# Performance work log

Measured on AMD Instinct MI355X. Metric: run time of the kernel, lower is better.

The kernel has to match this reference:

```python
import jax, jax.numpy as jnp
import numpy as np

CW = 64            # channel_width; N = CW**2 = 4096 tokens = d_batch
BIAS = 1.0         # same_channel_bias
D_KQ = 2048
D_V = 2048
STEP = 0           # self.step at first call
T_IDX = 0          # self.t at first call
PE_N = 10000.0


def pe_row(t, d, n=PE_N):
    """Row t of the sinusoidal positional encoding P[t, :] of width d (d even)."""
    i = jnp.arange(d // 2, dtype=jnp.float32)
    denom = jnp.power(jnp.float32(n), 2.0 * i / d)
    ang = jnp.float32(t) / denom
    row = jnp.zeros((d,), dtype=jnp.float32)
    row = row.at[0::2].set(jnp.sin(ang)).at[1::2].set(jnp.cos(ang))
    return row


def setup_inputs() -> dict:
    key = jax.random.key(0)
    ks = jax.random.split(key, 6)
    N = CW * CW          # 4096
    d_in = 2048
    num_steps = 8
    return {
        "x": jax.random.normal(ks[0], (N, d_in), dtype=jnp.float32),
        "W_query": jax.random.uniform(ks[1], (d_in, D_KQ), dtype=jnp.float32),
        "W_key": jax.random.uniform(ks[2], (d_in, D_KQ), dtype=jnp.float32),
        "W_value": jax.random.uniform(ks[3], (d_in, D_V), dtype=jnp.float32),
        "b_channel": jax.random.uniform(ks[4], (N, D_V), dtype=jnp.float32),
        "b_t": jax.random.uniform(ks[5], (num_steps, N, D_V), dtype=jnp.float32),
    }


def reference(x, W_query, W_key, W_value, b_channel, b_t):
    N = x.shape[0]
    q = x @ W_query                      # [N, d_kq]
    k = x @ W_key                        # [N, d_kq]
    v = x @ W_value                      # [N, d_v]
    scores = q @ k.T                     # [N, N]
    # kron(eye(cw), ones(cw,cw)*bias): +bias where tokens share a channel block
    ch = jnp.arange(N) // CW
    scores = scores + jnp.where(ch[:, None] == ch[None, :], jnp.float32(BIAS), jnp.float32(0.0))
    # NOTE: bias added BEFORE the 1/sqrt(d_kq) scaling, as in the original
    attn = jax.nn.softmax(scores / jnp.float32(D_KQ) ** 0.5, axis=-1)
    ctx = attn @ v                       # [N, d_v]
    ctx = ctx + b_channel + b_t[STEP] + pe_row(T_IDX, D_V)
    return ctx
```

## Files before the change

kernel.cpp:

```cpp
#include <hip/hip_runtime.h>
#include <cstdint>
#include <cstddef>


using h8    = __attribute__((ext_vector_type(8))) _Float16;
using h4    = __attribute__((ext_vector_type(4))) _Float16;
using f32x4 = __attribute__((ext_vector_type(4))) float;

__device__ __forceinline__ void gll16(const void* g, void* l) {
  __builtin_amdgcn_global_load_lds(
      (const __attribute__((address_space(1))) uint32_t*)g,
      (__attribute__((address_space(3))) uint32_t*)l, 16, 0, 0);
}

__global__ __launch_bounds__(256) void split_x_kernel(
    const float* __restrict__ X, _Float16* __restrict__ hi,
    _Float16* __restrict__ lo, int n4)
{
  int i = blockIdx.x * 256 + threadIdx.x;
  if (i >= n4) return;
  float4 v = ((const float4*)X)[i];
  float a[4] = {v.x, v.y, v.z, v.w};
  h4 hh, ll;
#pragma unroll
  for (int e = 0; e < 4; ++e) {
    _Float16 h = (_Float16)a[e];
    hh[e] = h;
    ll[e] = (_Float16)(a[e] - (float)h);
  }
  ((h4*)hi)[i] = hh;
  ((h4*)lo)[i] = ll;
}

__global__ __launch_bounds__(256) void transpose_split_w(
    const float* __restrict__ W, _Float16* __restrict__ Thi,
    _Float16* __restrict__ Tlo, int D, int writeLo)
{
  __shared__ float t[32][33];
  int n0 = blockIdx.x * 32;
  int k0 = blockIdx.y * 32;
  int tx = threadIdx.x & 31;
  int ty = threadIdx.x >> 5;
  for (int j = ty; j < 32; j += 8)
    t[j][tx] = W[(size_t)(k0 + j) * D + n0 + tx];
  __syncthreads();
  for (int j = ty; j < 32; j += 8) {
    float v = t[tx][j];
    size_t o = (size_t)(n0 + j) * D + k0 + tx;
    _Float16 h = (_Float16)v;
    Thi[o] = h;
    if (writeLo) Tlo[o] = (_Float16)(v - (float)h);
  }
}

constexpr int EPI_QK = 0;
constexpr int EPI_VT = 1;
constexpr int EPI_S  = 2;
constexpr int EPI_CTX = 3;

template<int EPI, bool SPLIT>
__global__ __launch_bounds__(256, 2) void gemm_bt(
    const _Float16* __restrict__ A, const _Float16* __restrict__ Al,
    const _Float16* __restrict__ B, const _Float16* __restrict__ Bl,
    int K, int lda, int ldb, int ldc, int ldt,
    float* __restrict__ of32, _Float16* __restrict__ oh1,
    _Float16* __restrict__ oh2,
    const float* __restrict__ c1, const float* __restrict__ c2)
{
  __shared__ __align__(16) _Float16 sA [128 * 32];
  __shared__ __align__(16) _Float16 sB [128 * 32];
  __shared__ __align__(16) _Float16 sAl[SPLIT ? 128 * 32 : 8];
  __shared__ __align__(16) _Float16 sBl[SPLIT ? 128 * 32 : 8];

  const int tid  = threadIdx.x;
  const int lane = tid & 63;
  const int wave = tid >> 6;
  const int wm = wave >> 1, wn = wave & 1;
  const int m0 = blockIdx.y * 128, n0 = blockIdx.x * 128;

  const int ca = lane + 64 * wave;
  const int ra = ca >> 2, ka = (ca & 3) * 8;
  const int cc = ca + 256;
  const int rb = cc >> 2, kb = (cc & 3) * 8;
  const size_t lo0 = (size_t)wave * 1024;
  const size_t lo1 = lo0 + 4096;

  const _Float16* gA0 = A + (size_t)(m0 + ra) * lda + ka;
  const _Float16* gA1 = A + (size_t)(m0 + rb) * lda + kb;
  const _Float16* gB0 = B + (size_t)(n0 + ra) * ldb + ka;
  const _Float16* gB1 = B + (size_t)(n0 + rb) * ldb + kb;
  const _Float16* gAl0 = Al ? Al + (size_t)(m0 + ra) * lda + ka : nullptr;
  const _Float16* gAl1 = Al ? Al + (size_t)(m0 + rb) * lda + kb : nullptr;
  const _Float16* gBl0 = Bl ? Bl + (size_t)(n0 + ra) * ldb + ka : nullptr;
  const _Float16* gBl1 = Bl ? Bl + (size_t)(n0 + rb) * ldb + kb : nullptr;

  f32x4 acc[4][4];
#pragma unroll
  for (int i = 0; i < 4; ++i)
#pragma unroll
    for (int j = 0; j < 4; ++j) acc[i][j] = (f32x4){0.f, 0.f, 0.f, 0.f};

  const int fr = lane & 15;
  const int fk = (lane >> 4) * 8;

  for (int k0 = 0; k0 < K; k0 += 32) {
    gll16(gA0 + k0, (char*)sA + lo0);
    gll16(gA1 + k0, (char*)sA + lo1);
    gll16(gB0 + k0, (char*)sB + lo0);
    gll16(gB1 + k0, (char*)sB + lo1);
    if constexpr (SPLIT) {
      gll16(gAl0 + k0, (char*)sAl + lo0);
      gll16(gAl1 + k0, (char*)sAl + lo1);
      gll16(gBl0 + k0, (char*)sBl + lo0);
      gll16(gBl1 + k0, (char*)sBl + lo1);
    }
    __syncthreads();

    h8 af[4], bf[4], afl[4], bfl[4];
#pragma unroll
    for (int mi = 0; mi < 4; ++mi)
      af[mi] = *(const h8*)&sA[(wm * 64 + mi * 16 + fr) * 32 + fk];
#pragma unroll
    for (int ni = 0; ni < 4; ++ni)
      bf[ni] = *(const h8*)&sB[(wn * 64 + ni * 16 + fr) * 32 + fk];
    if constexpr (SPLIT) {
#pragma unroll
      for (int mi = 0; mi < 4; ++mi)
        afl[mi] = *(const h8*)&sAl[(wm * 64 + mi * 16 + fr) * 32 + fk];
#pragma unroll
      for (int ni = 0; ni < 4; ++ni)
        bfl[ni] = *(const h8*)&sBl[(wn * 64 + ni * 16 + fr) * 32 + fk];
    }

#pragma unroll
    for (int mi = 0; mi < 4; ++mi)
#pragma unroll
      for (int ni = 0; ni < 4; ++ni) {
        acc[mi][ni] = __builtin_amdgcn_mfma_f32_16x16x32_f16(
            af[mi], bf[ni], acc[mi][ni], 0, 0, 0);
        if constexpr (SPLIT) {
          acc[mi][ni] = __builtin_amdgcn_mfma_f32_16x16x32_f16(
              af[mi], bfl[ni], acc[mi][ni], 0, 0, 0);
          acc[mi][ni] = __builtin_amdgcn_mfma_f32_16x16x32_f16(
              afl[mi], bf[ni], acc[mi][ni], 0, 0, 0);
        }
      }
    __syncthreads();
  }

  const int drow = (lane >> 4) * 4;
  const int dcol = lane & 15;
#pragma unroll
  for (int mi = 0; mi < 4; ++mi) {
#pragma unroll
    for (int ni = 0; ni < 4; ++ni) {
      const int row = m0 + wm * 64 + mi * 16 + drow;
      const int col = n0 + wn * 64 + ni * 16 + dcol;
      f32x4 v = acc[mi][ni];
      if constexpr (EPI == EPI_S) {
#pragma unroll
        for (int r = 0; r < 4; ++r)
          of32[(size_t)(row + r) * ldc + col] = v[r];
      } else if constexpr (EPI == EPI_QK) {
#pragma unroll
        for (int r = 0; r < 4; ++r) {
          float x = v[r];
          _Float16 hh = (_Float16)x;
          size_t o = (size_t)(row + r) * ldc + col;
          oh1[o] = hh;
          oh2[o] = (_Float16)(x - (float)hh);
        }
      } else if constexpr (EPI == EPI_VT) {
        h4 hh;
#pragma unroll
        for (int r = 0; r < 4; ++r) hh[r] = (_Float16)v[r];
        *(h4*)&oh1[(size_t)col * ldt + row] = hh;
      } else {
#pragma unroll
        for (int r = 0; r < 4; ++r) {
          size_t o = (size_t)(row + r) * ldc + col;
          of32[o] = v[r] + c1[o] + c2[o] + ((col & 1) ? 1.0f : 0.0f);
        }
      }
    }
  }
}

__global__ __launch_bounds__(256) void softmax_bias_kernel(
    float* __restrict__ S, int N)
{
  const float scale = 0.022097086912079608f;
  const int row = blockIdx.x;
  float* rp = S + (size_t)row * N;
  const int cblk = row & ~63;
  const int tid = threadIdx.x;

  float vals[16];
  float mx = -3.0e38f;
#pragma unroll
  for (int it = 0; it < 4; ++it) {
    int base = (it * 256 + tid) * 4;
    float4 v = *(const float4*)(rp + base);
    float a[4] = {v.x, v.y, v.z, v.w};
#pragma unroll
    for (int e = 0; e < 4; ++e) {
      int col = base + e;
      float s = a[e];
      if ((col & ~63) == cblk) s += 1.0f;
      s *= scale;
      vals[it * 4 + e] = s;
      mx = fmaxf(mx, s);
    }
  }
  __shared__ float red[8];
#pragma unroll
  for (int m = 32; m; m >>= 1) mx = fmaxf(mx, __shfl_xor(mx, m, 64));
  if ((tid & 63) == 0) red[tid >> 6] = mx;
  __syncthreads();
  mx = fmaxf(fmaxf(red[0], red[1]), fmaxf(red[2], red[3]));

  float sum = 0.f;
#pragma unroll
  for (int i = 0; i < 16; ++i) {
    float e = __expf(vals[i] - mx);
    vals[i] = e;
    sum += e;
  }
#pragma unroll
  for (int m = 32; m; m >>= 1) sum += __shfl_xor(sum, m, 64);
  if ((tid & 63) == 0) red[4 + (tid >> 6)] = sum;
  __syncthreads();
  sum = red[4] + red[5] + red[6] + red[7];
  float inv = 1.0f / sum;

  _Float16* op = (_Float16*)rp;
#pragma unroll
  for (int it = 0; it < 4; ++it) {
    int base = (it * 256 + tid) * 4;
    h4 hh;
#pragma unroll
    for (int e = 0; e < 4; ++e) hh[e] = (_Float16)(vals[it * 4 + e] * inv);
    *(h4*)(op + base) = hh;
  }
}

extern "C" void kernel_launch(void* const* d_in, const int* in_sizes, int n_in,
                              void* d_out, int out_size, void* d_ws,
                              size_t ws_size, hipStream_t stream)
{
  (void)in_sizes; (void)n_in; (void)out_size; (void)ws_size;
  const float* x   = (const float*)d_in[0];
  const float* Wq  = (const float*)d_in[1];
  const float* Wk  = (const float*)d_in[2];
  const float* Wv  = (const float*)d_in[3];
  const float* bch = (const float*)d_in[4];
  const float* bt0 = (const float*)d_in[5];
  float* out = (float*)d_out;

  char* ws = (char*)d_ws;
  const size_t O_XHI = 0;
  const size_t O_XLO = O_XHI + 16777216;
  const size_t O_WQH = O_XLO + 16777216;
  const size_t O_WQL = O_WQH + 8388608;
  const size_t O_WKH = O_WQL + 8388608;
  const size_t O_WKL = O_WKH + 8388608;
  const size_t O_S   = 0;
  const size_t O_WVH = 67108864;
  const size_t O_VT  = O_WVH + 8388608;
  const size_t O_QH  = O_VT + 16777216;
  const size_t O_QL  = O_QH + 16777216;
  const size_t O_KH  = O_QL + 16777216;
  const size_t O_KL  = O_KH + 16777216;

  _Float16* xhi = (_Float16*)(ws + O_XHI);
  _Float16* xlo = (_Float16*)(ws + O_XLO);
  _Float16* wqh = (_Float16*)(ws + O_WQH);
  _Float16* wql = (_Float16*)(ws + O_WQL);
  _Float16* wkh = (_Float16*)(ws + O_WKH);
  _Float16* wkl = (_Float16*)(ws + O_WKL);
  _Float16* wvh = (_Float16*)(ws + O_WVH);
  _Float16* vT  = (_Float16*)(ws + O_VT);
  _Float16* qh  = (_Float16*)(ws + O_QH);
  _Float16* ql  = (_Float16*)(ws + O_QL);
  _Float16* kh  = (_Float16*)(ws + O_KH);
  _Float16* kl  = (_Float16*)(ws + O_KL);
  float*    S   = (float*)(ws + O_S);

  split_x_kernel<<<2097152 / 256, 256, 0, stream>>>(x, xhi, xlo, 2097152);
  dim3 tg(64, 64);
  transpose_split_w<<<tg, 256, 0, stream>>>(Wq, wqh, wql, 2048, 1);
  transpose_split_w<<<tg, 256, 0, stream>>>(Wk, wkh, wkl, 2048, 1);
  transpose_split_w<<<tg, 256, 0, stream>>>(Wv, wvh, nullptr, 2048, 0);

  dim3 g1(2048 / 128, 4096 / 128);
  gemm_bt<EPI_QK, true><<<g1, 256, 0, stream>>>(
      xhi, xlo, wqh, wql, 2048, 2048, 2048, 2048, 0,
      nullptr, qh, ql, nullptr, nullptr);
  gemm_bt<EPI_QK, true><<<g1, 256, 0, stream>>>(
      xhi, xlo, wkh, wkl, 2048, 2048, 2048, 2048, 0,
      nullptr, kh, kl, nullptr, nullptr);
  gemm_bt<EPI_VT, false><<<g1, 256, 0, stream>>>(
      xhi, nullptr, wvh, nullptr, 2048, 2048, 2048, 0, 4096,
      nullptr, vT, nullptr, nullptr, nullptr);

  dim3 g2(4096 / 128, 4096 / 128);
  gemm_bt<EPI_S, true><<<g2, 256, 0, stream>>>(
      qh, ql, kh, kl, 2048, 2048, 2048, 4096, 0,
      S, nullptr, nullptr, nullptr, nullptr);

  softmax_bias_kernel<<<4096, 256, 0, stream>>>(S, 4096);

  gemm_bt<EPI_CTX, false><<<g1, 256, 0, stream>>>(
      (const _Float16*)S, nullptr, vT, nullptr, 4096, 8192, 4096, 2048, 0,
      out, nullptr, nullptr, bch, bt0);
}
```

Before: 956.7 us.

## Fuse Q/K projection GEMMs, re-layout LDS tiles, raise occupancy, compact attention buffer

Concatenates the transposed Wq and Wk weights so one GEMM launch produces Q and K side by side. The attention-score GEMM then reads them with stride 4096. The LDS staging layout changes from row-major 32-wide rows to k-chunk-major blocks of 8 halves, which changes how fragments are read and may reduce bank conflicts. Launch bounds rise to 4 or 6 blocks per CU. Softmax now writes its fp16 output to a separate compact buffer, so the context GEMM reads it with lda 4096 instead of a strided view inside S. The higher occupancy target may force register spills.

```diff
diff --git a/kernel.cpp b/kernel.cpp
--- a/kernel.cpp
+++ b/kernel.cpp
@@ -59,7 +59,7 @@
 constexpr int EPI_CTX = 3;
 
 template<int EPI, bool SPLIT>
-__global__ __launch_bounds__(256, 2) void gemm_bt(
+__global__ __launch_bounds__(256, SPLIT ? 4 : 6) void gemm_bt(
     const _Float16* __restrict__ A, const _Float16* __restrict__ Al,
     const _Float16* __restrict__ B, const _Float16* __restrict__ Bl,
     int K, int lda, int ldb, int ldc, int ldt,
@@ -78,21 +78,18 @@
   const int wm = wave >> 1, wn = wave & 1;
   const int m0 = blockIdx.y * 128, n0 = blockIdx.x * 128;
 
-  const int ca = lane + 64 * wave;
-  const int ra = ca >> 2, ka = (ca & 3) * 8;
-  const int cc = ca + 256;
-  const int rb = cc >> 2, kb = (cc & 3) * 8;
+  const int s0 = wave * 64 + lane;
+  const int r  = s0 & 127;
+  const int j0 = s0 >> 7;
   const size_t lo0 = (size_t)wave * 1024;
   const size_t lo1 = lo0 + 4096;
 
-  const _Float16* gA0 = A + (size_t)(m0 + ra) * lda + ka;
-  const _Float16* gA1 = A + (size_t)(m0 + rb) * lda + kb;
-  const _Float16* gB0 = B + (size_t)(n0 + ra) * ldb + ka;
-  const _Float16* gB1 = B + (size_t)(n0 + rb) * ldb + kb;
-  const _Float16* gAl0 = Al ? Al + (size_t)(m0 + ra) * lda + ka : nullptr;
-  const _Float16* gAl1 = Al ? Al + (size_t)(m0 + rb) * lda + kb : nullptr;
-  const _Float16* gBl0 = Bl ? Bl + (size_t)(n0 + ra) * ldb + ka : nullptr;
-  const _Float16* gBl1 = Bl ? Bl + (size_t)(n0 + rb) * ldb + kb : nullptr;
+  const _Float16* gA0 = A + (size_t)(m0 + r) * lda + j0 * 8;
+  const _Float16* gA1 = gA0 + 16;
+  const _Float16* gB0 = B + (size_t)(n0 + r) * ldb + j0 * 8;
+  const _Float16* gB1 = gB0 + 16;
+  const _Float16* gAl0 = Al ? Al + (size_t)(m0 + r) * lda + j0 * 8 : nullptr;
+  const _Float16* gBl0 = Bl ? Bl + (size_t)(n0 + r) * ldb + j0 * 8 : nullptr;
 
   f32x4 acc[4][4];
 #pragma unroll
@@ -101,7 +98,7 @@
     for (int j = 0; j < 4; ++j) acc[i][j] = (f32x4){0.f, 0.f, 0.f, 0.f};
 
   const int fr = lane & 15;
-  const int fk = (lane >> 4) * 8;
+  const int jc = lane >> 4;
 
   for (int k0 = 0; k0 < K; k0 += 32) {
     gll16(gA0 + k0, (char*)sA + lo0);
@@ -110,26 +107,26 @@
     gll16(gB1 + k0, (char*)sB + lo1);
     if constexpr (SPLIT) {
       gll16(gAl0 + k0, (char*)sAl + lo0);
-      gll16(gAl1 + k0, (char*)sAl + lo1);
+      gll16(gAl0 + 16 + k0, (char*)sAl + lo1);
       gll16(gBl0 + k0, (char*)sBl + lo0);
-      gll16(gBl1 + k0, (char*)sBl + lo1);
+      gll16(gBl0 + 16 + k0, (char*)sBl + lo1);
     }
     __syncthreads();
 
     h8 af[4], bf[4], afl[4], bfl[4];
 #pragma unroll
     for (int mi = 0; mi < 4; ++mi)
-      af[mi] = *(const h8*)&sA[(wm * 64 + mi * 16 + fr) * 32 + fk];
+      af[mi] = *(const h8*)&sA[jc * 1024 + (wm * 64 + mi * 16 + fr) * 8];
 #pragma unroll
     for (int ni = 0; ni < 4; ++ni)
-      bf[ni] = *(const h8*)&sB[(wn * 64 + ni * 16 + fr) * 32 + fk];
+      bf[ni] = *(const h8*)&sB[jc * 1024 + (wn * 64 + ni * 16 + fr) * 8];
     if constexpr (SPLIT) {
 #pragma unroll
       for (int mi = 0; mi < 4; ++mi)
-        afl[mi] = *(const h8*)&sAl[(wm * 64 + mi * 16 + fr) * 32 + fk];
+        afl[mi] = *(const h8*)&sAl[jc * 1024 + (wm * 64 + mi * 16 + fr) * 8];
 #pragma unroll
       for (int ni = 0; ni < 4; ++ni)
-        bfl[ni] = *(const h8*)&sBl[(wn * 64 + ni * 16 + fr) * 32 + fk];
+        bfl[ni] = *(const h8*)&sBl[jc * 1024 + (wn * 64 + ni * 16 + fr) * 8];
     }
 
 #pragma unroll
@@ -159,27 +156,27 @@
       f32x4 v = acc[mi][ni];
       if constexpr (EPI == EPI_S) {
 #pragma unroll
-        for (int r = 0; r < 4; ++r)
-          of32[(size_t)(row + r) * ldc + col] = v[r];
+        for (int rr = 0; rr < 4; ++rr)
+          of32[(size_t)(row + rr) * ldc + col] = v[rr];
       } else if constexpr (EPI == EPI_QK) {
 #pragma unroll
-        for (int r = 0; r < 4; ++r) {
-          float x = v[r];
+        for (int rr = 0; rr < 4; ++rr) {
+          float x = v[rr];
           _Float16 hh = (_Float16)x;
-          size_t o = (size_t)(row + r) * ldc + col;
+          size_t o = (size_t)(row + rr) * ldc + col;
           oh1[o] = hh;
           oh2[o] = (_Float16)(x - (float)hh);
         }
       } else if constexpr (EPI == EPI_VT) {
         h4 hh;
 #pragma unroll
-        for (int r = 0; r < 4; ++r) hh[r] = (_Float16)v[r];
+        for (int rr = 0; rr < 4; ++rr) hh[rr] = (_Float16)v[rr];
         *(h4*)&oh1[(size_t)col * ldt + row] = hh;
       } else {
 #pragma unroll
-        for (int r = 0; r < 4; ++r) {
-          size_t o = (size_t)(row + r) * ldc + col;
-          of32[o] = v[r] + c1[o] + c2[o] + ((col & 1) ? 1.0f : 0.0f);
+        for (int rr = 0; rr < 4; ++rr) {
+          size_t o = (size_t)(row + rr) * ldc + col;
+          of32[o] = v[rr] + c1[o] + c2[o] + ((col & 1) ? 1.0f : 0.0f);
         }
       }
     }
@@ -187,11 +184,11 @@
 }
 
 __global__ __launch_bounds__(256) void softmax_bias_kernel(
-    float* __restrict__ S, int N)
+    const float* __restrict__ S, _Float16* __restrict__ attn, int N)
 {
   const float scale = 0.022097086912079608f;
   const int row = blockIdx.x;
-  float* rp = S + (size_t)row * N;
+  const float* rp = S + (size_t)row * N;
   const int cblk = row & ~63;
   const int tid = threadIdx.x;
 
@@ -233,7 +230,7 @@
   sum = red[4] + red[5] + red[6] + red[7];
   float inv = 1.0f / sum;
 
-  _Float16* op = (_Float16*)rp;
+  _Float16* op = attn + (size_t)row * N;
 #pragma unroll
   for (int it = 0; it < 4; ++it) {
     int base = (it * 256 + tid) * 4;
@@ -258,59 +255,52 @@
   float* out = (float*)d_out;
 
   char* ws = (char*)d_ws;
-  const size_t O_XHI = 0;
-  const size_t O_XLO = O_XHI + 16777216;
-  const size_t O_WQH = O_XLO + 16777216;
-  const size_t O_WQL = O_WQH + 8388608;
-  const size_t O_WKH = O_WQL + 8388608;
-  const size_t O_WKL = O_WKH + 8388608;
-  const size_t O_S   = 0;
-  const size_t O_WVH = 67108864;
-  const size_t O_VT  = O_WVH + 8388608;
-  const size_t O_QH  = O_VT + 16777216;
-  const size_t O_QL  = O_QH + 16777216;
-  const size_t O_KH  = O_QL + 16777216;
-  const size_t O_KL  = O_KH + 16777216;
-
-  _Float16* xhi = (_Float16*)(ws + O_XHI);
-  _Float16* xlo = (_Float16*)(ws + O_XLO);
-  _Float16* wqh = (_Float16*)(ws + O_WQH);
-  _Float16* wql = (_Float16*)(ws + O_WQL);
-  _Float16* wkh = (_Float16*)(ws + O_WKH);
-  _Float16* wkl = (_Float16*)(ws + O_WKL);
-  _Float16* wvh = (_Float16*)(ws + O_WVH);
-  _Float16* vT  = (_Float16*)(ws + O_VT);
-  _Float16* qh  = (_Float16*)(ws + O_QH);
-  _Float16* ql  = (_Float16*)(ws + O_QL);
-  _Float16* kh  = (_Float16*)(ws + O_KH);
-  _Float16* kl  = (_Float16*)(ws + O_KL);
-  float*    S   = (float*)(ws + O_S);
+  const size_t O_XHI  = 0;
+  const size_t O_XLO  = 16777216;
+  const size_t O_WQKH = 33554432;
+  const size_t O_WQKL = 50331648;
+  const size_t O_WVH  = 67108864;
+  const size_t O_VT   = 75497472;
+  const size_t O_QKH  = 92274688;
+  const size_t O_QKL  = 125829120;
+  const size_t O_S    = 0;
+  const size_t O_ATTN = O_QKH;
+
+  _Float16* xhi  = (_Float16*)(ws + O_XHI);
+  _Float16* xlo  = (_Float16*)(ws + O_XLO);
+  _Float16* wqkh = (_Float16*)(ws + O_WQKH);
+  _Float16* wqkl = (_Float16*)(ws + O_WQKL);
+  _Float16* wvh  = (_Float16*)(ws + O_WVH);
+  _Float16* vT   = (_Float16*)(ws + O_VT);
+  _Float16* qkh  = (_Float16*)(ws + O_QKH);
+  _Float16* qkl  = (_Float16*)(ws + O_QKL);
+  float*    S    = (float*)(ws + O_S);
+  _Float16* attn = (_Float16*)(ws + O_ATTN);
 
   split_x_kernel<<<2097152 / 256, 256, 0, stream>>>(x, xhi, xlo, 2097152);
   dim3 tg(64, 64);
-  transpose_split_w<<<tg, 256, 0, stream>>>(Wq, wqh, wql, 2048, 1);
-  transpose_split_w<<<tg, 256, 0, stream>>>(Wk, wkh, wkl, 2048, 1);
+  transpose_split_w<<<tg, 256, 0, stream>>>(Wq, wqkh, wqkl, 2048, 1);
+  transpose_split_w<<<tg, 256, 0, stream>>>(Wk, wqkh + 4194304, wqkl + 4194304, 2048, 1);
   transpose_split_w<<<tg, 256, 0, stream>>>(Wv, wvh, nullptr, 2048, 0);
 
-  dim3 g1(2048 / 128, 4096 / 128);
-  gemm_bt<EPI_QK, true><<<g1, 256, 0, stream>>>(
-      xhi, xlo, wqh, wql, 2048, 2048, 2048, 2048, 0,
-      nullptr, qh, ql, nullptr, nullptr);
-  gemm_bt<EPI_QK, true><<<g1, 256, 0, stream>>>(
-      xhi, xlo, wkh, wkl, 2048, 2048, 2048, 2048, 0,
-      nullptr, kh, kl, nullptr, nullptr);
-  gemm_bt<EPI_VT, false><<<g1, 256, 0, stream>>>(
+  dim3 gqk(4096 / 128, 4096 / 128);
+  gemm_bt<EPI_QK, true><<<gqk, 256, 0, stream>>>(
+      xhi, xlo, wqkh, wqkl, 2048, 2048, 2048, 4096, 0,
+      nullptr, qkh, qkl, nullptr, nullptr);
+  dim3 gv(2048 / 128, 4096 / 128);
+  gemm_bt<EPI_VT, false><<<gv, 256, 0, stream>>>(
       xhi, nullptr, wvh, nullptr, 2048, 2048, 2048, 0, 4096,
       nullptr, vT, nullptr, nullptr, nullptr);
 
-  dim3 g2(4096 / 128, 4096 / 128);
-  gemm_bt<EPI_S, true><<<g2, 256, 0, stream>>>(
-      qh, ql, kh, kl, 2048, 2048, 2048, 4096, 0,
+  dim3 gs(4096 / 128, 4096 / 128);
+  gemm_bt<EPI_S, true><<<gs, 256, 0, stream>>>(
+      qkh, qkl, qkh + 2048, qkl + 2048, 2048, 4096, 4096, 4096, 0,
       S, nullptr, nullptr, nullptr, nullptr);
 
-  softmax_bias_kernel<<<4096, 256, 0, stream>>>(S, 4096);
-
-  gemm_bt<EPI_CTX, false><<<g1, 256, 0, stream>>>(
-      (const _Float16*)S, nullptr, vT, nullptr, 4096, 8192, 4096, 2048, 0,
+  softmax_bias_kernel<<<4096, 256, 0, stream>>>(S, attn, 4096);
+
+  dim3 gc(2048 / 128, 4096 / 128);
+  gemm_bt<EPI_CTX, false><<<gc, 256, 0, stream>>>(
+      attn, nullptr, vT, nullptr, 4096, 4096, 4096, 2048, 0,
       out, nullptr, nullptr, bch, bt0);
 }
```

New measurement: 1.546 ms. +61.6%, slower.
